# Optimization experiments

Hardware: AMD Instinct MI355X
Metric: run time of the kernel (lower is better)

## Reference

```python
import jax, jax.numpy as jnp
import numpy as np

V, E, U, B, T = 50000, 256, 512, 256, 256  # vocab, embed, units, batch, seq_len


def setup_inputs() -> dict:
    key = jax.random.key(0)
    ks = jax.random.split(key, 10)
    tokens = jax.random.randint(ks[0], (B, T), 0, V)
    emb = jax.random.normal(ks[1], (V, E), dtype=jnp.float32) * 0.02
    s_e = 1.0 / np.sqrt(E)
    s_u = 1.0 / np.sqrt(U)
    W0 = jax.random.normal(ks[2], (E, 4 * U), dtype=jnp.float32) * s_e
    U0 = jax.random.normal(ks[3], (U, 4 * U), dtype=jnp.float32) * s_u
    b0 = jnp.zeros((4 * U,), dtype=jnp.float32)
    W1 = jax.random.normal(ks[4], (U, 4 * U), dtype=jnp.float32) * s_u
    U1 = jax.random.normal(ks[5], (U, 4 * U), dtype=jnp.float32) * s_u
    b1 = jnp.zeros((4 * U,), dtype=jnp.float32)
    Wd = jax.random.normal(ks[6], (U, 1), dtype=jnp.float32) * s_u
    bd = jnp.zeros((1,), dtype=jnp.float32)
    return {"tokens": tokens, "emb": emb, "W0": W0, "U0": U0, "b0": b0,
            "W1": W1, "U1": U1, "b1": b1, "Wd": Wd, "bd": bd}


def _lstm_gates(z, c):
    # Keras gate order: i, f, g (candidate), o
    i, f, g, o = jnp.split(z, 4, axis=-1)
    c_new = jax.nn.sigmoid(f) * c + jax.nn.sigmoid(i) * jnp.tanh(g)
    h_new = jax.nn.sigmoid(o) * jnp.tanh(c_new)
    return h_new, c_new


def reference(tokens, emb, W0, U0, b0, W1, U1, b1, Wd, bd):
    x = emb[tokens]  # [B, T, E]
    # Precompute input projections for layer 0 in one big GEMM: [T, B, 4U]
    xz0 = jnp.einsum('bte,ef->tbf', x, W0) + b0

    h0 = jnp.zeros((tokens.shape[0], U0.shape[0]), dtype=x.dtype)
    c0 = jnp.zeros_like(h0)
    h1 = jnp.zeros_like(h0)
    c1 = jnp.zeros_like(h0)

    def step(carry, xz_t):
        h0, c0, h1, c1 = carry
        h0, c0 = _lstm_gates(xz_t + h0 @ U0, c0)
        h1, c1 = _lstm_gates(h0 @ W1 + h1 @ U1 + b1, c1)
        return (h0, c0, h1, c1), None

    (h0, c0, h1, c1), _ = jax.lax.scan(step, (h0, c0, h1, c1), xz0)
    return jax.nn.sigmoid(h1 @ Wd + bd)  # [B, 1]
```

## Files before the change

### kernel.cpp

```cpp
#include <hip/hip_runtime.h>
#include <hip/hip_bf16.h>
#include <math.h>

#define VB 50000
#define EE 256
#define UU 512
#define BB 256
#define TT 256
#define G4 2048

typedef __attribute__((ext_vector_type(8))) short short8;
typedef __attribute__((ext_vector_type(2))) unsigned long long u64x2;
typedef __attribute__((ext_vector_type(4))) float f32x4;

__device__ __forceinline__ float sigf(float x){ return 1.0f/(1.0f+expf(-x)); }
__device__ __forceinline__ unsigned short f2bf(float f){
    __hip_bfloat16 h = __float2bfloat16(f);
    unsigned short s; __builtin_memcpy(&s,&h,2); return s;
}
__device__ __forceinline__ float bf2f(unsigned short u){
    unsigned int x = ((unsigned int)u)<<16; float f; __builtin_memcpy(&f,&x,4); return f;
}

__device__ __forceinline__ unsigned int cldu(const unsigned int* p){
    return __hip_atomic_load(p, __ATOMIC_RELAXED, __HIP_MEMORY_SCOPE_AGENT);
}
__device__ __forceinline__ void cstu(unsigned int* p, unsigned int v){
    __hip_atomic_store(p, v, __ATOMIC_RELAXED, __HIP_MEMORY_SCOPE_AGENT);
}

__device__ __forceinline__ short8 cld16c(const unsigned short* p){
    short8 v;
    asm volatile("global_load_dwordx4 %0, %1, off"
                 : "=&v"(v) : "v"(p));
    return v;
}
__device__ __forceinline__ void cst16w(unsigned long long* dp, u64x2 v){
    asm volatile("global_store_dwordx4 %0, %1, off sc1"
                 :: "v"(dp), "v"(v) : "memory");
}

__global__ __launch_bounds__(256) void wtrans(const float* __restrict__ in, int rows,
                                              unsigned short* __restrict__ out,
                                              int Kout, int koff) {
    __shared__ float tl[32][33];
    int tx = threadIdx.x, ty = threadIdx.y;
    int c0 = blockIdx.x * 32, k0 = blockIdx.y * 32;
    #pragma unroll
    for (int i = 0; i < 4; i++)
        tl[ty + i * 8][tx] = in[(size_t)(k0 + ty + i * 8) * G4 + c0 + tx];
    __syncthreads();
    #pragma unroll
    for (int i = 0; i < 4; i++)
        out[(size_t)(c0 + ty + i * 8) * Kout + koff + k0 + tx] = f2bf(tl[tx][ty + i * 8]);
}

__global__ __launch_bounds__(64) void xgather(const int* __restrict__ tokens,
                                              const float* __restrict__ emb,
                                              unsigned short* __restrict__ xbf) {
    int flat = blockIdx.x;
    int b = flat & 255, t = flat >> 8;
    int tok = tokens[b * TT + t];
    float4 v = ((const float4*)(emb + (size_t)tok * EE))[threadIdx.x];
    ushort4 o;
    o.x = f2bf(v.x); o.y = f2bf(v.y); o.z = f2bf(v.z); o.w = f2bf(v.w);
    ((ushort4*)(xbf + ((size_t)t * BB + b) * EE))[threadIdx.x] = o;
}

__global__ __launch_bounds__(256, 1) void rnn_persist(
    const unsigned short* __restrict__ Wt0,
    const unsigned short* __restrict__ Wt1,
    const unsigned short* __restrict__ xbf,
    const int* __restrict__ tokens, const float* __restrict__ emb,
    const float* __restrict__ b0v, const float* __restrict__ b1v,
    unsigned short* __restrict__ h0buf,
    unsigned short* __restrict__ h1buf,
    unsigned int* __restrict__ bars,
    int use_xbf)
{
    extern __shared__ char smem[];
    unsigned short* wl  = (unsigned short*)smem;
    unsigned short* hst = (unsigned short*)(smem + 131072);
    int*            tokl = (int*)(smem + 131072 + 3072);

    const int tid   = threadIdx.x;
    const int bid   = blockIdx.x;
    const int g     = bid >> 6;
    const int local = bid & 63;
    const int layer = local >> 5;
    const int u0    = (local & 31) * 16;
    const int row0  = g * 64;
    const int K     = layer ? 1024 : 768;
    const int KT    = K / 32;
    const unsigned short* Wt = layer ? Wt1 : Wt0;
    const float* bR = layer ? b1v : b0v;

    const int nch = 4 * KT * 64;
    for (int i = tid; i < nch; i += 256) {
        int n  = i & 15;
        int q2 = (i >> 4) & 3;
        int t2 = i >> 6;
        int kt = t2 % KT, gate = t2 / KT;
        const unsigned short* src = Wt + (size_t)(gate * UU + u0 + n) * K + kt * 32 + q2 * 8;
        *(short8*)(wl + (size_t)i * 8) = *(const short8*)src;
    }

    float gb[4];
    #pragma unroll
    for (int gate = 0; gate < 4; gate++) gb[gate] = bR[gate * UU + u0 + (tid & 15)];
    float cst[4] = {0.f, 0.f, 0.f, 0.f};

    const int lane = tid & 63;
    const int w    = tid >> 6;
    const int n16  = lane & 15;
    const int q    = lane >> 4;
    const int q8   = q * 8;
    const int myrow = row0 + w * 16 + n16;
    const unsigned short* wlane = wl + lane * 8;

    unsigned int* flg = bars + (size_t)g * 1024;
    unsigned int* myFlag = flg + local;
    const unsigned int* pollp = flg + lane;

    const size_t HS = (size_t)BB * UU;

    __syncthreads();

    for (int p = 0; p <= TT; p++) {
        if ((p & 7) == 0)
            __builtin_amdgcn_fence(__ATOMIC_ACQUIRE, "agent");

        f32x4 acc[4];
        #pragma unroll
        for (int gate = 0; gate < 4; gate++)
            acc[gate] = (f32x4){gb[gate], gb[gate], gb[gate], gb[gate]};

        short8 xv[8];
        if (layer == 0 && p < TT) {
            if (!use_xbf) {
                if (tid < 64) tokl[tid] = tokens[(size_t)(row0 + tid) * TT + p];
                __syncthreads();
                const float* ep = emb + (size_t)tokl[w * 16 + n16] * EE + q8;
                #pragma unroll
                for (int kt = 0; kt < 8; kt++) {
                    float4 f0 = *(const float4*)(ep + kt * 32);
                    float4 f1 = *(const float4*)(ep + kt * 32 + 4);
                    union { unsigned short s[8]; short8 v; } u;
                    u.s[0]=f2bf(f0.x); u.s[1]=f2bf(f0.y); u.s[2]=f2bf(f0.z); u.s[3]=f2bf(f0.w);
                    u.s[4]=f2bf(f1.x); u.s[5]=f2bf(f1.y); u.s[6]=f2bf(f1.z); u.s[7]=f2bf(f1.w);
                    #pragma unroll
                    for (int gate = 0; gate < 4; gate++) {
                        short8 bv = *(const short8*)(wlane + (size_t)(gate * KT + kt) * 512);
                        acc[gate] = __builtin_amdgcn_mfma_f32_16x16x32_bf16(u.v, bv, acc[gate], 0, 0, 0);
                    }
                }
            } else {
                const unsigned short* xp = xbf + ((size_t)p * BB + myrow) * EE + q8;
                #pragma unroll
                for (int kt = 0; kt < 8; kt++)
                    xv[kt] = *(const short8*)(xp + kt * 32);
            }
        }

        if (layer == 0) {
            if (p < TT) {
                if (tid < 64) {
                    for (;;) {
                        bool bad = (lane < 32) && ((int)cldu(pollp) < p);
                        if (__ballot(bad) == 0ULL) break;
                        __builtin_amdgcn_s_sleep(1);
                    }
                }
                __syncthreads();

                const unsigned short* h0r = h0buf + (size_t)(p & 15) * HS;
                unsigned short* hw = h0buf + (size_t)((p + 1) & 15) * HS;
                const unsigned short* ah = h0r + (size_t)myrow * UU + q8;
                short8 hb[16];
                #pragma unroll
                for (int i = 0; i < 16; i++) hb[i] = cld16c(ah + i * 32);
                if (use_xbf) {
                    #pragma unroll
                    for (int kt = 0; kt < 8; kt++) {
                        #pragma unroll
                        for (int gate = 0; gate < 4; gate++) {
                            short8 bv = *(const short8*)(wlane + (size_t)(gate * KT + kt) * 512);
                            acc[gate] = __builtin_amdgcn_mfma_f32_16x16x32_bf16(xv[kt], bv, acc[gate], 0, 0, 0);
                        }
                    }
                }
                asm volatile("s_waitcnt vmcnt(0)" ::: "memory");
                __builtin_amdgcn_sched_barrier(0);
                #pragma unroll
                for (int i = 0; i < 16; i++) {
                    #pragma unroll
                    for (int gate = 0; gate < 4; gate++) {
                        short8 bv = *(const short8*)(wlane + (size_t)(gate * KT + 8 + i) * 512);
                        acc[gate] = __builtin_amdgcn_mfma_f32_16x16x32_bf16(hb[i], bv, acc[gate], 0, 0, 0);
                    }
                }

                #pragma unroll
                for (int r = 0; r < 4; r++) {
                    float zi = acc[0][r];
                    float zf = acc[1][r];
                    float zg = acc[2][r];
                    float zo = acc[3][r];
                    float cn = sigf(zf) * cst[r] + sigf(zi) * tanhf(zg);
                    cst[r] = cn;
                    hst[(w * 16 + q * 4 + r) * 24 + n16] = f2bf(sigf(zo) * tanhf(cn));
                }
                __syncthreads();

                {
                    const int thr = p - 6;
                    if (thr > 0) {
                        for (;;) {
                            bool bad = (lane >= 32) && ((int)cldu(pollp) < thr);
                            if (__ballot(bad) == 0ULL) break;
                            __builtin_amdgcn_s_sleep(1);
                        }
                    }
                }
                if (tid < 128) {
                    int row = tid >> 1, half = tid & 1;
                    u64x2 sv = *(const u64x2*)(hst + row * 24 + half * 8);
                    unsigned long long* dp = (unsigned long long*)
                        (hw + (size_t)(row0 + row) * UU + u0 + half * 8);
                    cst16w(dp, sv);
                }
            }
        } else {
            if (p >= 1) {
                const unsigned short* h0r = h0buf + (size_t)(p & 15) * HS;
                const unsigned short* h1r = h1buf + (size_t)((p - 1) & 15) * HS;
                unsigned short* hw = h1buf + (size_t)(p & 15) * HS;
                const unsigned short* a0 = h0r + (size_t)myrow * UU + q8;
                const unsigned short* a1 = h1r + (size_t)myrow * UU + q8;

                for (;;) {
                    bool bad = (lane < 32) && ((int)cldu(pollp) < p);
                    if (__ballot(bad) == 0ULL) break;
                    __builtin_amdgcn_s_sleep(1);
                }
                short8 ha[16];
                #pragma unroll
                for (int i = 0; i < 16; i++) ha[i] = cld16c(a0 + i * 32);

                for (;;) {
                    bool bad = (lane >= 32) && ((int)cldu(pollp) < p);
                    if (__ballot(bad) == 0ULL) break;
                    __builtin_amdgcn_s_sleep(1);
                }
                short8 hc[16];
                #pragma unroll
                for (int i = 0; i < 16; i++) hc[i] = cld16c(a1 + i * 32);

                asm volatile("s_waitcnt vmcnt(16)" ::: "memory");
                __builtin_amdgcn_sched_barrier(0);
                #pragma unroll
                for (int i = 0; i < 16; i++) {
                    #pragma unroll
                    for (int gate = 0; gate < 4; gate++) {
                        short8 bv = *(const short8*)(wlane + (size_t)(gate * KT + i) * 512);
                        acc[gate] = __builtin_amdgcn_mfma_f32_16x16x32_bf16(ha[i], bv, acc[gate], 0, 0, 0);
                    }
                }
                asm volatile("s_waitcnt vmcnt(0)" ::: "memory");
                __builtin_amdgcn_sched_barrier(0);
                #pragma unroll
                for (int i = 0; i < 16; i++) {
                    #pragma unroll
                    for (int gate = 0; gate < 4; gate++) {
                        short8 bv = *(const short8*)(wlane + (size_t)(gate * KT + 16 + i) * 512);
                        acc[gate] = __builtin_amdgcn_mfma_f32_16x16x32_bf16(hc[i], bv, acc[gate], 0, 0, 0);
                    }
                }

                #pragma unroll
                for (int r = 0; r < 4; r++) {
                    float zi = acc[0][r];
                    float zf = acc[1][r];
                    float zg = acc[2][r];
                    float zo = acc[3][r];
                    float cn = sigf(zf) * cst[r] + sigf(zi) * tanhf(zg);
                    cst[r] = cn;
                    hst[(w * 16 + q * 4 + r) * 24 + n16] = f2bf(sigf(zo) * tanhf(cn));
                }
                __syncthreads();
                if (tid < 128) {
                    int row = tid >> 1, half = tid & 1;
                    u64x2 sv = *(const u64x2*)(hst + row * 24 + half * 8);
                    unsigned long long* dp = (unsigned long long*)
                        (hw + (size_t)(row0 + row) * UU + u0 + half * 8);
                    cst16w(dp, sv);
                }
            }
        }

        if (p < TT) {
            asm volatile("s_waitcnt vmcnt(0)" ::: "memory");
            __syncthreads();
            if (tid == 0) cstu(myFlag, (unsigned int)(p + 1));
        }
    }
}

__global__ __launch_bounds__(64) void dense_out(
    const unsigned short* __restrict__ h, const float* __restrict__ Wd,
    const float* __restrict__ bd, float* __restrict__ out)
{
    int b = blockIdx.x;
    int lane = threadIdx.x;
    float s = 0.f;
    #pragma unroll
    for (int k = lane; k < UU; k += 64) s += bf2f(h[(size_t)b * UU + k]) * Wd[k];
    #pragma unroll
    for (int off = 32; off > 0; off >>= 1) s += __shfl_down(s, off);
    if (lane == 0) out[b] = sigf(s + bd[0]);
}

extern "C" void kernel_launch(void* const* d_in, const int* in_sizes, int n_in,
                              void* d_out, int out_size, void* d_ws, size_t ws_size,
                              hipStream_t stream) {
    const int*   tokens = (const int*)  d_in[0];
    const float* emb    = (const float*)d_in[1];
    const float* W0     = (const float*)d_in[2];
    const float* U0     = (const float*)d_in[3];
    const float* b0     = (const float*)d_in[4];
    const float* W1     = (const float*)d_in[5];
    const float* U1     = (const float*)d_in[6];
    const float* b1     = (const float*)d_in[7];
    const float* Wd     = (const float*)d_in[8];
    const float* bd     = (const float*)d_in[9];
    float* out = (float*)d_out;

    const size_t SLOT = (size_t)BB * UU * 2;
    const size_t oWt0 = 0;
    const size_t oWt1 = (size_t)G4 * 768 * 2;
    const size_t oH0  = oWt1 + (size_t)G4 * 1024 * 2;
    const size_t oH1  = oH0 + 16 * SLOT;
    const size_t oBar = oH1 + 16 * SLOT;
    const size_t oX   = oBar + 32768;
    const size_t needFull = oX + (size_t)TT * BB * EE * 2;
    int use_xbf = (ws_size >= needFull) ? 1 : 0;

    unsigned short* Wt0p = (unsigned short*)((char*)d_ws + oWt0);
    unsigned short* Wt1p = (unsigned short*)((char*)d_ws + oWt1);
    unsigned short* h0p  = (unsigned short*)((char*)d_ws + oH0);
    unsigned short* h1p  = (unsigned short*)((char*)d_ws + oH1);
    unsigned int*   barp = (unsigned int*)  ((char*)d_ws + oBar);
    unsigned short* xbfp = (unsigned short*)((char*)d_ws + oX);

    hipMemsetAsync(h0p, 0, SLOT, stream);
    hipMemsetAsync(h1p, 0, SLOT, stream);
    hipMemsetAsync(barp, 0, 32768, stream);

    wtrans<<<dim3(G4 / 32, EE / 32), dim3(32, 8), 0, stream>>>(W0, EE, Wt0p, 768, 0);
    wtrans<<<dim3(G4 / 32, UU / 32), dim3(32, 8), 0, stream>>>(U0, UU, Wt0p, 768, 256);
    wtrans<<<dim3(G4 / 32, UU / 32), dim3(32, 8), 0, stream>>>(W1, UU, Wt1p, 1024, 0);
    wtrans<<<dim3(G4 / 32, UU / 32), dim3(32, 8), 0, stream>>>(U1, UU, Wt1p, 1024, 512);

    if (use_xbf)
        xgather<<<dim3(BB * TT), dim3(64), 0, stream>>>(tokens, emb, xbfp);

    {
        const size_t shmem = 131072 + 3072 + 256;
        hipFuncSetAttribute((const void*)rnn_persist,
                            hipFuncAttributeMaxDynamicSharedMemorySize, (int)shmem);
        void* args[] = {(void*)&Wt0p, (void*)&Wt1p, (void*)&xbfp,
                        (void*)&tokens, (void*)&emb, (void*)&b0, (void*)&b1,
                        (void*)&h0p, (void*)&h1p, (void*)&barp, (void*)&use_xbf};
        hipLaunchCooperativeKernel((const void*)rnn_persist, dim3(256), dim3(256),
                                   args, shmem, stream);
    }

    dense_out<<<dim3(BB), dim3(64), 0, stream>>>(h1p, Wd, bd, out);
}
```

Measured before the change: 1.980 ms.

## Remap block roles across XCDs and add local-L2 fast paths for flags and h stores

Block-to-role mapping is permuted so each group of cooperating blocks lands on the same XCD (bid&7 selects the group). Flag polls first try a load with sc0 that may hit the local L2, and fall back to the coherent load. Hidden-state and flag stores are issued twice, once plain (local L2) and once with sc1, so same-XCD consumers can see data sooner. This targets cross-XCD synchronization latency in the persistent recurrent loop, at the cost of extra stores and reliance on dispatch order and cache-coherence behaviour.

```diff
diff --git a/kernel.cpp b/kernel.cpp
--- a/kernel.cpp
+++ b/kernel.cpp
@@ -28,6 +28,12 @@
 __device__ __forceinline__ void cstu(unsigned int* p, unsigned int v){
     __hip_atomic_store(p, v, __ATOMIC_RELAXED, __HIP_MEMORY_SCOPE_AGENT);
 }
+__device__ __forceinline__ unsigned int cldu_l2(const unsigned int* p){
+    unsigned int v;
+    asm volatile("global_load_dword %0, %1, off sc0\n\ts_waitcnt vmcnt(0)"
+                 : "=v"(v) : "v"(p) : "memory");
+    return v;
+}
 
 __device__ __forceinline__ short8 cld16c(const unsigned short* p){
     short8 v;
@@ -35,8 +41,9 @@
                  : "=&v"(v) : "v"(p));
     return v;
 }
-__device__ __forceinline__ void cst16w(unsigned long long* dp, u64x2 v){
-    asm volatile("global_store_dwordx4 %0, %1, off sc1"
+__device__ __forceinline__ void cst16dual(unsigned long long* dp, u64x2 v){
+    asm volatile("global_store_dwordx4 %0, %1, off\n\t"
+                 "global_store_dwordx4 %0, %1, off sc1"
                  :: "v"(dp), "v"(v) : "memory");
 }
 
@@ -85,8 +92,9 @@
 
     const int tid   = threadIdx.x;
     const int bid   = blockIdx.x;
-    const int g     = bid >> 6;
-    const int local = bid & 63;
+    const int role  = ((bid & 7) << 5) | (bid >> 3);
+    const int g     = role >> 6;
+    const int local = role & 63;
     const int layer = local >> 5;
     const int u0    = (local & 31) * 16;
     const int row0  = g * 64;
@@ -166,7 +174,9 @@
             if (p < TT) {
                 if (tid < 64) {
                     for (;;) {
-                        bool bad = (lane < 32) && ((int)cldu(pollp) < p);
+                        bool bad = (lane < 32) && ((int)cldu_l2(pollp) < p);
+                        if (__ballot(bad) == 0ULL) break;
+                        bad = (lane < 32) && ((int)cldu(pollp) < p);
                         if (__ballot(bad) == 0ULL) break;
                         __builtin_amdgcn_s_sleep(1);
                     }
@@ -216,7 +226,9 @@
                     const int thr = p - 6;
                     if (thr > 0) {
                         for (;;) {
-                            bool bad = (lane >= 32) && ((int)cldu(pollp) < thr);
+                            bool bad = (lane >= 32) && ((int)cldu_l2(pollp) < thr);
+                            if (__ballot(bad) == 0ULL) break;
+                            bad = (lane >= 32) && ((int)cldu(pollp) < thr);
                             if (__ballot(bad) == 0ULL) break;
                             __builtin_amdgcn_s_sleep(1);
                         }
@@ -227,7 +239,7 @@
                     u64x2 sv = *(const u64x2*)(hst + row * 24 + half * 8);
                     unsigned long long* dp = (unsigned long long*)
                         (hw + (size_t)(row0 + row) * UU + u0 + half * 8);
-                    cst16w(dp, sv);
+                    cst16dual(dp, sv);
                 }
             }
         } else {
@@ -239,7 +251,9 @@
                 const unsigned short* a1 = h1r + (size_t)myrow * UU + q8;
 
                 for (;;) {
-                    bool bad = (lane < 32) && ((int)cldu(pollp) < p);
+                    bool bad = (lane < 32) && ((int)cldu_l2(pollp) < p);
+                    if (__ballot(bad) == 0ULL) break;
+                    bad = (lane < 32) && ((int)cldu(pollp) < p);
                     if (__ballot(bad) == 0ULL) break;
                     __builtin_amdgcn_s_sleep(1);
                 }
@@ -248,7 +262,9 @@
                 for (int i = 0; i < 16; i++) ha[i] = cld16c(a0 + i * 32);
 
                 for (;;) {
-                    bool bad = (lane >= 32) && ((int)cldu(pollp) < p);
+                    bool bad = (lane >= 32) && ((int)cldu_l2(pollp) < p);
+                    if (__ballot(bad) == 0ULL) break;
+                    bad = (lane >= 32) && ((int)cldu(pollp) < p);
                     if (__ballot(bad) == 0ULL) break;
                     __builtin_amdgcn_s_sleep(1);
                 }
@@ -293,7 +309,7 @@
                     u64x2 sv = *(const u64x2*)(hst + row * 24 + half * 8);
                     unsigned long long* dp = (unsigned long long*)
                         (hw + (size_t)(row0 + row) * UU + u0 + half * 8);
-                    cst16w(dp, sv);
+                    cst16dual(dp, sv);
                 }
             }
         }
@@ -301,7 +317,12 @@
         if (p < TT) {
             asm volatile("s_waitcnt vmcnt(0)" ::: "memory");
             __syncthreads();
-            if (tid == 0) cstu(myFlag, (unsigned int)(p + 1));
+            if (tid == 0) {
+                unsigned int v = (unsigned int)(p + 1);
+                asm volatile("global_store_dword %0, %1, off"
+                             :: "v"(myFlag), "v"(v) : "memory");
+                cstu(myFlag, v);
+            }
         }
     }
 }
```

Measured after the change: 2.845 ms. 43.7% more time.
